# Optimization experiments

Hardware: AMD Instinct MI355X
Metric: run time of the kernel (lower is better)

## Reference

```python
import jax, jax.numpy as jnp
import numpy as np

B, S, H = 4, 1024, 1024
NH, HD = 16, 64          # heads, head_dim (NH*HD == H)
E, K, I = 8, 2, 1024     # routed experts, top_k, expert intermediate
NSH = 2                  # shared experts -> shared intermediate = NSH*I
EPS = 1e-6


def setup_inputs() -> dict:
    key = jax.random.key(0)
    ks = jax.random.split(key, 12)
    init = lambda k, shape: (jax.random.normal(k, shape, jnp.float32) * 0.02)
    return {
        "hidden_states": jax.random.normal(ks[0], (B, S, H), jnp.float32),
        "conditioning": jax.random.normal(ks[1], (B, H), jnp.float32),
        "adaLN_W": init(ks[2], (H, 6 * H)),
        "ln1_scale": jnp.ones((H,), jnp.float32),
        "ln1_bias": jnp.zeros((H,), jnp.float32),
        "ln2_scale": jnp.ones((H,), jnp.float32),
        "ln2_bias": jnp.zeros((H,), jnp.float32),
        "Wq": init(ks[3], (H, H)),
        "Wk": init(ks[4], (H, H)),
        "Wv": init(ks[5], (H, H)),
        "Wo": init(ks[6], (H, H)),
        "gate_kernel": init(ks[7], (E, H)),
        "We1": init(ks[8], (E, H, I)),
        "We2": init(ks[9], (E, I, H)),
        "Ws1": init(ks[10], (H, NSH * I)),
        "Ws2": init(ks[11], (NSH * I, H)),
    }


def _layernorm(x, scale, bias):
    m = x.mean(-1, keepdims=True)
    v = x.var(-1, keepdims=True)
    return (x - m) * jax.lax.rsqrt(v + EPS) * scale + bias


def _modulate(x, shift, scale):
    # (1 + scale) * x + shift, broadcasting [B,H] conditioning over seq dim
    return x * (1.0 + scale[:, None, :]) + shift[:, None, :]


def _attention(x, Wq, Wk, Wv, Wo):
    b, s, h = x.shape
    q = (x @ Wq).reshape(b, s, NH, HD)
    k = (x @ Wk).reshape(b, s, NH, HD)
    v = (x @ Wv).reshape(b, s, NH, HD)
    scores = jnp.einsum("bqnd,bknd->bnqk", q, k) / np.sqrt(HD).astype(np.float32)
    probs = jax.nn.softmax(scores, axis=-1)
    out = jnp.einsum("bnqk,bknd->bqnd", probs, v).reshape(b, s, h)
    return out @ Wo


def reference(hidden_states, conditioning, adaLN_W, ln1_scale, ln1_bias,
              ln2_scale, ln2_bias, Wq, Wk, Wv, Wo, gate_kernel, We1, We2,
              Ws1, Ws2):
    # adaLN modulation: SiLU -> Linear(H, 6H) -> chunk 6
    mods = jax.nn.silu(conditioning) @ adaLN_W  # [B, 6H]
    (shift_msa, scale_msa, gate_msa,
     shift_mlp, scale_mlp, gate_mlp) = jnp.split(mods, 6, axis=-1)

    normed = _modulate(_layernorm(hidden_states, ln1_scale, ln1_bias),
                       shift_msa, scale_msa)
    attn_out = _attention(normed, Wq, Wk, Wv, Wo)
    h = hidden_states + gate_msa[:, None, :] * attn_out

    normed2 = _modulate(_layernorm(h, ln2_scale, ln2_bias),
                        shift_mlp, scale_mlp)

    # --- MoE gate (DeepSeek-V2 style, greedy top-k, softmax scoring) ---
    logits = jnp.einsum("bsh,eh->bse", normed2.astype(jnp.float32),
                        gate_kernel.astype(jnp.float32))
    scores = jax.nn.softmax(logits, axis=-1)           # [B,S,E]
    topk_w, topk_idx = jax.lax.top_k(scores, K)        # [B,S,K]
    topk_w = topk_w / (topk_w.sum(-1, keepdims=True) + 1e-20)  # norm_topk_prob

    # --- dense all-expert MLPs then top-k combine (as in DiTMLPMoE) ---
    eh = jax.nn.gelu(jnp.einsum("bsh,ehi->ebsi", normed2, We1))  # [E,B,S,I]
    eo = jnp.einsum("ebsi,eih->bseh", eh, We2)                   # [B,S,E,H]
    sel = jnp.take_along_axis(eo, topk_idx[..., None], axis=2)   # [B,S,K,H]
    y = (sel * topk_w[..., None].astype(sel.dtype)).sum(axis=2)  # [B,S,H]

    # shared experts (always active)
    y = y + jax.nn.gelu(normed2 @ Ws1) @ Ws2

    return h + gate_mlp[:, None, :] * y
```

## Files before the change

kernel.cpp:

```cpp
#include <hip/hip_runtime.h>

typedef __bf16 bf16x8 __attribute__((ext_vector_type(8)));
typedef __bf16 bf16x4 __attribute__((ext_vector_type(4)));
typedef float  f32x4  __attribute__((ext_vector_type(4)));

__device__ inline float wred_sum(float v){
  #pragma unroll
  for (int d = 1; d < 64; d <<= 1) v += __shfl_xor(v, d, 64);
  return v;
}

__device__ inline float gelu_t(float x){
  const float c0 = 0.7978845608028654f;
  float t = tanhf(c0 * (x + 0.044715f * x * x * x));
  return 0.5f * x * (1.0f + t);
}

__device__ __forceinline__ void gload_lds16(const __bf16* g, __bf16* l){
  __builtin_amdgcn_global_load_lds((const __attribute__((address_space(1))) void*)g,
                                   (__attribute__((address_space(3))) void*)l, 16, 0, 0);
}

__global__ __launch_bounds__(256)
void transpose_cvt(const float* __restrict__ in, __bf16* __restrict__ out, int R, int C){
  long mo = (long)blockIdx.z * R * C;
  in += mo; out += mo;
  __shared__ float t[32][33];
  int r0 = blockIdx.y * 32, c0 = blockIdx.x * 32;
  int tid = threadIdx.x;
  int tr = tid >> 3, tc = (tid & 7) * 4;
  float4 vv = *(const float4*)&in[(long)(r0 + tr) * C + c0 + tc];
  t[tr][tc + 0] = vv.x; t[tr][tc + 1] = vv.y; t[tr][tc + 2] = vv.z; t[tr][tc + 3] = vv.w;
  __syncthreads();
  int oc = tid >> 3, orr = (tid & 7) * 4;
  bf16x4 o4;
  #pragma unroll
  for (int i = 0; i < 4; i++) o4[i] = (__bf16)t[orr + i][oc];
  *(bf16x4*)&out[(long)(c0 + oc) * R + r0 + orr] = o4;
}

__global__ __launch_bounds__(256)
void adaln_k(const float* __restrict__ cond, const float* __restrict__ W, float* __restrict__ mods){
  int b = blockIdx.y, z = blockIdx.z;
  int col = (blockIdx.x * 256 + threadIdx.x) * 4;
  __shared__ float sc[256];
  int h2 = z * 256 + threadIdx.x;
  float x = cond[b * 1024 + h2];
  sc[threadIdx.x] = x / (1.f + expf(-x));
  __syncthreads();
  float a0 = 0.f, a1 = 0.f, a2 = 0.f, a3 = 0.f;
  #pragma unroll 4
  for (int i = 0; i < 256; i++){
    float s = sc[i];
    float4 wv = *(const float4*)&W[(long)(z * 256 + i) * 6144 + col];
    a0 += s * wv.x; a1 += s * wv.y; a2 += s * wv.z; a3 += s * wv.w;
  }
  atomicAdd(&mods[b * 6144 + col + 0], a0);
  atomicAdd(&mods[b * 6144 + col + 1], a1);
  atomicAdd(&mods[b * 6144 + col + 2], a2);
  atomicAdd(&mods[b * 6144 + col + 3], a3);
}

__global__ __launch_bounds__(256)
void ln_mod(const float* __restrict__ x, const float* __restrict__ sc, const float* __restrict__ bi,
            const float* __restrict__ mods, int shift_off, int scale_off, __bf16* __restrict__ out){
  int row = blockIdx.x, tid = threadIdx.x, b = row >> 10;
  float4 xv = *(const float4*)&x[(long)row * 1024 + tid * 4];
  float s  = xv.x + xv.y + xv.z + xv.w;
  float s2 = xv.x * xv.x + xv.y * xv.y + xv.z * xv.z + xv.w * xv.w;
  s = wred_sum(s); s2 = wred_sum(s2);
  __shared__ float ssum[4], ssum2[4];
  int w = tid >> 6;
  if ((tid & 63) == 0){ ssum[w] = s; ssum2[w] = s2; }
  __syncthreads();
  s = ssum[0] + ssum[1] + ssum[2] + ssum[3];
  s2 = ssum2[0] + ssum2[1] + ssum2[2] + ssum2[3];
  float mean = s * (1.f / 1024.f);
  float var  = s2 * (1.f / 1024.f) - mean * mean;
  float inv  = rsqrtf(var + 1e-6f);
  const float xa[4] = {xv.x, xv.y, xv.z, xv.w};
  #pragma unroll
  for (int i = 0; i < 4; i++){
    int c = tid * 4 + i;
    float nv = (xa[i] - mean) * inv * sc[c] + bi[c];
    nv = nv * (1.f + mods[b * 6144 + scale_off + c]) + mods[b * 6144 + shift_off + c];
    out[(long)row * 1024 + c] = (__bf16)nv;
  }
}

__global__ __launch_bounds__(256)
void gate_k(const float* __restrict__ h, const float* __restrict__ ln2s, const float* __restrict__ ln2b,
            const float* __restrict__ mods, const float* __restrict__ gw,
            int* __restrict__ eidx, float* __restrict__ wpair){
  __shared__ float gws[8192];
  int tid = threadIdx.x;
  #pragma unroll
  for (int i = 0; i < 8; i++){
    int idx = tid + i * 256;
    *(float4*)&gws[idx * 4] = *(const float4*)&gw[idx * 4];
  }
  __syncthreads();
  int wv = tid >> 6, lane = tid & 63;
  int tok = blockIdx.x * 4 + wv;
  int b = tok >> 10;
  float4 xv[4]; float s = 0.f, s2 = 0.f;
  #pragma unroll
  for (int ch = 0; ch < 4; ch++){
    float4 v = *(const float4*)&h[(long)tok * 1024 + ch * 256 + lane * 4];
    xv[ch] = v;
    s  += v.x + v.y + v.z + v.w;
    s2 += v.x * v.x + v.y * v.y + v.z * v.z + v.w * v.w;
  }
  s = wred_sum(s); s2 = wred_sum(s2);
  float mean = s * (1.f / 1024.f);
  float var  = s2 * (1.f / 1024.f) - mean * mean;
  float inv  = rsqrtf(var + 1e-6f);
  float lg[8];
  #pragma unroll
  for (int e = 0; e < 8; e++) lg[e] = 0.f;
  #pragma unroll
  for (int ch = 0; ch < 4; ch++){
    int c = ch * 256 + lane * 4;
    float4 s4  = *(const float4*)&ln2s[c];
    float4 b4  = *(const float4*)&ln2b[c];
    float4 sc4 = *(const float4*)&mods[b * 6144 + 4096 + c];
    float4 sh4 = *(const float4*)&mods[b * 6144 + 3072 + c];
    float n0 = ((xv[ch].x - mean) * inv * s4.x + b4.x) * (1.f + sc4.x) + sh4.x;
    float n1 = ((xv[ch].y - mean) * inv * s4.y + b4.y) * (1.f + sc4.y) + sh4.y;
    float n2 = ((xv[ch].z - mean) * inv * s4.z + b4.z) * (1.f + sc4.z) + sh4.z;
    float n3 = ((xv[ch].w - mean) * inv * s4.w + b4.w) * (1.f + sc4.w) + sh4.w;
    #pragma unroll
    for (int e = 0; e < 8; e++){
      float4 g4 = *(const float4*)&gws[e * 1024 + c];
      lg[e] += n0 * g4.x + n1 * g4.y + n2 * g4.z + n3 * g4.w;
    }
  }
  #pragma unroll
  for (int e = 0; e < 8; e++) lg[e] = wred_sum(lg[e]);
  if (lane == 0){
    float mx = lg[0];
    #pragma unroll
    for (int e = 1; e < 8; e++) mx = fmaxf(mx, lg[e]);
    float p[8], ss = 0.f;
    #pragma unroll
    for (int e = 0; e < 8; e++){ p[e] = expf(lg[e] - mx); ss += p[e]; }
    #pragma unroll
    for (int e = 0; e < 8; e++) p[e] /= ss;
    int i0 = 0; float b0 = p[0];
    #pragma unroll
    for (int e = 1; e < 8; e++) if (p[e] > b0){ b0 = p[e]; i0 = e; }
    int i1 = -1; float b1 = -1.f;
    #pragma unroll
    for (int e = 0; e < 8; e++) if (e != i0 && p[e] > b1){ b1 = p[e]; i1 = e; }
    float dn = b0 + b1 + 1e-20f;
    eidx[tok * 2]     = i0; wpair[tok * 2]     = b0 / dn;
    eidx[tok * 2 + 1] = i1; wpair[tok * 2 + 1] = b1 / dn;
  }
}

__global__ __launch_bounds__(256)
void build_k(const int* __restrict__ eidx, int* __restrict__ counts, int* __restrict__ lists){
  int e = blockIdx.x;
  int tid = threadIdx.x, wv = tid >> 6, lane = tid & 63;
  __shared__ int base;
  __shared__ int woff[4];
  if (tid == 0) base = 0;
  __syncthreads();
  for (int it = 0; it < 32; ++it){
    int i = it * 256 + tid;
    bool m = (eidx[i] == e);
    unsigned long long bal = __ballot(m);
    int prefix = __popcll(bal & ((1ull << lane) - 1ull));
    if (lane == 0) woff[wv] = __popcll(bal);
    __syncthreads();
    int off = base;
    #pragma unroll
    for (int k = 0; k < 4; k++) if (k < wv) off += woff[k];
    if (m) lists[e * 4096 + off + prefix] = i;
    __syncthreads();
    if (tid == 0) base += woff[0] + woff[1] + woff[2] + woff[3];
    __syncthreads();
  }
  if (tid == 0) counts[e] = base;
}

__global__ __launch_bounds__(256)
void attn_k(const __bf16* __restrict__ qkv, __bf16* __restrict__ og){
  int bh = blockIdx.y; int bb = bh >> 4, hn = bh & 15;
  int q0 = blockIdx.x * 64;
  long tokbase = (long)bb * 1024;
  int hd0 = hn * 64;
  int tid = threadIdx.x; int w = tid >> 6; int lane = tid & 63;

  __shared__ __bf16 Ks[64][72];
  __shared__ __bf16 Vt[64][72];
  __shared__ __bf16 Ps[4][16][72];

  long qrow = tokbase + q0 + w * 16 + (lane & 15);
  bf16x8 qf0 = *(const bf16x8*)&qkv[qrow * 3072 + hd0 + (lane >> 4) * 8];
  bf16x8 qf1 = *(const bf16x8*)&qkv[qrow * 3072 + hd0 + 32 + (lane >> 4) * 8];
  #pragma unroll
  for (int i = 0; i < 8; i++){
    qf0[i] = (__bf16)((float)qf0[i] * 0.125f);
    qf1[i] = (__bf16)((float)qf1[i] * 0.125f);
  }

  float m_r[4], l_r[4];
  f32x4 oa[4];
  #pragma unroll
  for (int r = 0; r < 4; r++){ m_r[r] = -1e30f; l_r[r] = 0.f; }
  #pragma unroll
  for (int hb = 0; hb < 4; hb++) oa[hb] = (f32x4){0.f, 0.f, 0.f, 0.f};

  int dcol = tid & 63, rblk = tid >> 6;
  for (int t = 0; t < 16; t++){
    long kvbase = tokbase + t * 64;
    #pragma unroll
    for (int p = 0; p < 2; p++){
      int r = (tid >> 3) + p * 32;
      int c = (tid & 7) * 8;
      *(bf16x8*)&Ks[r][c] = *(const bf16x8*)&qkv[(kvbase + r) * 3072 + 1024 + hd0 + c];
    }
    bf16x8 col0, col1;
    #pragma unroll
    for (int i = 0; i < 8; i++)
      col0[i] = qkv[(kvbase + rblk * 16 + i) * 3072 + 2048 + hd0 + dcol];
    #pragma unroll
    for (int i = 0; i < 8; i++)
      col1[i] = qkv[(kvbase + rblk * 16 + 8 + i) * 3072 + 2048 + hd0 + dcol];
    *(bf16x8*)&Vt[dcol][rblk * 16]     = col0;
    *(bf16x8*)&Vt[dcol][rblk * 16 + 8] = col1;
    __syncthreads();
    f32x4 sf[4];
    #pragma unroll
    for (int cb = 0; cb < 4; cb++){
      bf16x8 kf0 = *(const bf16x8*)&Ks[cb * 16 + (lane & 15)][(lane >> 4) * 8];
      bf16x8 kf1 = *(const bf16x8*)&Ks[cb * 16 + (lane & 15)][32 + (lane >> 4) * 8];
      f32x4 sacc = (f32x4){0.f, 0.f, 0.f, 0.f};
      sacc = __builtin_amdgcn_mfma_f32_16x16x32_bf16(qf0, kf0, sacc, 0, 0, 0);
      sacc = __builtin_amdgcn_mfma_f32_16x16x32_bf16(qf1, kf1, sacc, 0, 0, 0);
      sf[cb] = sacc;
    }
    #pragma unroll
    for (int r = 0; r < 4; r++){
      float mx = fmaxf(fmaxf(sf[0][r], sf[1][r]), fmaxf(sf[2][r], sf[3][r]));
      #pragma unroll
      for (int d = 1; d < 16; d <<= 1) mx = fmaxf(mx, __shfl_xor(mx, d, 64));
      float mn = fmaxf(m_r[r], mx);
      float fr = expf(m_r[r] - mn);
      m_r[r] = mn;
      float ps = 0.f;
      #pragma unroll
      for (int cb = 0; cb < 4; cb++){
        float pe = expf(sf[cb][r] - mn);
        sf[cb][r] = pe;
        ps += pe;
      }
      #pragma unroll
      for (int d = 1; d < 16; d <<= 1) ps += __shfl_xor(ps, d, 64);
      l_r[r] = l_r[r] * fr + ps;
      #pragma unroll
      for (int hb = 0; hb < 4; hb++) oa[hb][r] *= fr;
    }
    #pragma unroll
    for (int cb = 0; cb < 4; cb++)
      #pragma unroll
      for (int r = 0; r < 4; r++)
        Ps[w][(lane >> 4) * 4 + r][cb * 16 + (lane & 15)] = (__bf16)sf[cb][r];
    __syncthreads();
    bf16x8 pf0 = *(const bf16x8*)&Ps[w][lane & 15][(lane >> 4) * 8];
    bf16x8 pf1 = *(const bf16x8*)&Ps[w][lane & 15][32 + (lane >> 4) * 8];
    #pragma unroll
    for (int hb = 0; hb < 4; hb++){
      bf16x8 vf0 = *(const bf16x8*)&Vt[hb * 16 + (lane & 15)][(lane >> 4) * 8];
      bf16x8 vf1 = *(const bf16x8*)&Vt[hb * 16 + (lane & 15)][32 + (lane >> 4) * 8];
      oa[hb] = __builtin_amdgcn_mfma_f32_16x16x32_bf16(pf0, vf0, oa[hb], 0, 0, 0);
      oa[hb] = __builtin_amdgcn_mfma_f32_16x16x32_bf16(pf1, vf1, oa[hb], 0, 0, 0);
    }
    __syncthreads();
  }
  #pragma unroll
  for (int hb = 0; hb < 4; hb++)
    #pragma unroll
    for (int r = 0; r < 4; r++){
      long row = tokbase + q0 + w * 16 + (lane >> 4) * 4 + r;
      float val = oa[hb][r] / l_r[r];
      og[row * 1024 + hd0 + hb * 16 + (lane & 15)] = (__bf16)val;
    }
}

template<int EPI, int GMODE>
__global__ __launch_bounds__(256)
void gemm_k(const __bf16* __restrict__ A, int lda,
            const __bf16* __restrict__ Bt, int K, long bstride,
            const int* __restrict__ lists, const int* __restrict__ counts,
            __bf16* __restrict__ outb, int ldo,
            float* __restrict__ outf,
            const float* __restrict__ resid,
            const float* __restrict__ mods, int mod_off,
            const float* __restrict__ wpair){
  int e = blockIdx.z;
  int cnt = 1 << 30;
  const int* list = nullptr;
  if (GMODE){
    cnt = counts[e];
    if ((int)blockIdx.y * 128 >= cnt) return;
    list = lists + e * 4096;
    Bt += (long)e * bstride;
  }
  int row0 = blockIdx.y * 128;
  int n0 = blockIdx.x * 128;
  int tid = threadIdx.x;
  int lane = tid & 63, w = tid >> 6;
  int wr = (w >> 1) * 64, wc = (w & 1) * 64;

  __shared__ __bf16 As[128 * 64];
  __shared__ __bf16 Bs[128 * 64];

  f32x4 acc[4][4];
  #pragma unroll
  for (int m = 0; m < 4; m++)
    #pragma unroll
    for (int n = 0; n < 4; n++) acc[m][n] = (f32x4){0.f, 0.f, 0.f, 0.f};

  long aoff[4]; const __bf16* bptr[4];
  #pragma unroll
  for (int j = 0; j < 4; j++){
    int r = w * 32 + j * 8 + (lane >> 3);
    int scb = (lane & 7) ^ (r & 7);
    int gr = row0 + r;
    int srcr;
    if (GMODE == 0) srcr = gr;
    else if (gr < cnt){ int pv = list[gr]; srcr = (GMODE == 1) ? (pv >> 1) : pv; }
    else { int pv = list[0]; srcr = (GMODE == 1) ? (pv >> 1) : pv; }
    aoff[j] = (long)srcr * lda + scb * 8;
    bptr[j] = Bt + (long)(n0 + r) * K + scb * 8;
  }
  const int nk = K / 64;
  for (int kt = 0; kt < nk; ++kt){
    int k0 = kt * 64;
    #pragma unroll
    for (int j = 0; j < 4; j++){
      gload_lds16(A + aoff[j] + k0, &As[(w * 32 + j * 8) * 64]);
      gload_lds16(bptr[j] + k0,     &Bs[(w * 32 + j * 8) * 64]);
    }
    __syncthreads();
    #pragma unroll
    for (int ks = 0; ks < 2; ++ks){
      bf16x8 af[4], bfr[4];
      #pragma unroll
      for (int m = 0; m < 4; m++){
        int r = wr + m * 16 + (lane & 15);
        int blk = (ks * 4 + (lane >> 4)) ^ (r & 7);
        af[m] = *(const bf16x8*)&As[r * 64 + blk * 8];
      }
      #pragma unroll
      for (int n = 0; n < 4; n++){
        int r = wc + n * 16 + (lane & 15);
        int blk = (ks * 4 + (lane >> 4)) ^ (r & 7);
        bfr[n] = *(const bf16x8*)&Bs[r * 64 + blk * 8];
      }
      #pragma unroll
      for (int m = 0; m < 4; m++)
        #pragma unroll
        for (int n = 0; n < 4; n++)
          acc[m][n] = __builtin_amdgcn_mfma_f32_16x16x32_bf16(af[m], bfr[n], acc[m][n], 0, 0, 0);
    }
    __syncthreads();
  }
  #pragma unroll
  for (int m = 0; m < 4; m++){
    #pragma unroll
    for (int r = 0; r < 4; r++){
      int rl = wr + m * 16 + (lane >> 4) * 4 + r;
      int grow = row0 + rl;
      if (GMODE && grow >= cnt) continue;
      #pragma unroll
      for (int n = 0; n < 4; n++){
        int col = n0 + wc + n * 16 + (lane & 15);
        float v = acc[m][n][r];
        if (EPI == 0){
          outb[(long)grow * ldo + col] = (__bf16)v;
        } else if (EPI == 1){
          int dst = (GMODE == 1) ? list[grow] : grow;
          outb[(long)dst * ldo + col] = (__bf16)gelu_t(v);
        } else if (EPI == 2){
          int b = grow >> 10;
          outf[(long)grow * 1024 + col] = resid[(long)grow * 1024 + col] + mods[b * 6144 + mod_off + col] * v;
        } else if (EPI == 3){
          outf[(long)grow * 1024 + col] = v;
        } else if (EPI == 4){
          int pv = list[grow];
          atomicAdd(&outf[(long)(pv >> 1) * 1024 + col], wpair[pv] * v);
        }
      }
    }
  }
}

__global__ __launch_bounds__(256)
void final_k(const float* __restrict__ h, const float* __restrict__ y,
             const float* __restrict__ mods, float* __restrict__ out){
  int i = blockIdx.x * 256 + threadIdx.x;
  long base = (long)i * 4;
  int row = (int)(base >> 10); int b = row >> 10; int c = (int)(base & 1023);
  float4 hv = *(const float4*)&h[base];
  float4 yv = *(const float4*)&y[base];
  const float* g = &mods[b * 6144 + 5120 + c];
  float4 o;
  o.x = hv.x + g[0] * yv.x;
  o.y = hv.y + g[1] * yv.y;
  o.z = hv.z + g[2] * yv.z;
  o.w = hv.w + g[3] * yv.w;
  *(float4*)&out[base] = o;
}

extern "C" void kernel_launch(void* const* d_in, const int* in_sizes, int n_in,
                              void* d_out, int out_size, void* d_ws, size_t ws_size,
                              hipStream_t stream){
  const float* hidden = (const float*)d_in[0];
  const float* cond   = (const float*)d_in[1];
  const float* adaW   = (const float*)d_in[2];
  const float* ln1s   = (const float*)d_in[3];
  const float* ln1b   = (const float*)d_in[4];
  const float* ln2s   = (const float*)d_in[5];
  const float* ln2b   = (const float*)d_in[6];
  const float* Wq     = (const float*)d_in[7];
  const float* Wk     = (const float*)d_in[8];
  const float* Wv     = (const float*)d_in[9];
  const float* Wo     = (const float*)d_in[10];
  const float* gatek  = (const float*)d_in[11];
  const float* We1    = (const float*)d_in[12];
  const float* We2    = (const float*)d_in[13];
  const float* Ws1    = (const float*)d_in[14];
  const float* Ws2    = (const float*)d_in[15];
  float* out = (float*)d_out;

  const size_t MB = 1024 * 1024;
  char* W = (char*)d_ws;
  size_t off = 0;
  auto take = [&](size_t b) -> void* {
    void* p = W + off;
    off += (b + 255) & ~((size_t)255);
    return p;
  };
  float*  mods   = (float*) take(4 * 6144 * sizeof(float));
  __bf16* qkvT   = (__bf16*)take(6 * MB);
  __bf16* WoT    = (__bf16*)take(2 * MB);
  __bf16* Ws1T   = (__bf16*)take(4 * MB);
  __bf16* Ws2T   = (__bf16*)take(4 * MB);
  __bf16* We1T   = (__bf16*)take(16 * MB);
  __bf16* We2T   = (__bf16*)take(16 * MB);
  __bf16* n1     = (__bf16*)take(8 * MB);
  __bf16* ab     = (__bf16*)take(8 * MB);
  __bf16* qkv    = (__bf16*)take(24 * MB);
  float*  hb     = (float*) take(16 * MB);
  __bf16* n2     = (__bf16*)take(8 * MB);
  float*  yb     = (float*) take(16 * MB);
  int*    counts = (int*)   take(256);
  int*    lists  = (int*)   take(8 * 4096 * 4);
  float*  wpair  = (float*) take(8192 * 4);
  int*    eidx   = (int*)   take(8192 * 4);
  __bf16* EH = n1;
  __bf16* SH = qkv;

  dim3 blk(256);

  hipMemsetAsync(mods, 0, 4 * 6144 * sizeof(float), stream);

  transpose_cvt<<<dim3(32, 32, 1), blk, 0, stream>>>(Wq,  qkvT,              1024, 1024);
  transpose_cvt<<<dim3(32, 32, 1), blk, 0, stream>>>(Wk,  qkvT + 1024*1024,  1024, 1024);
  transpose_cvt<<<dim3(32, 32, 1), blk, 0, stream>>>(Wv,  qkvT + 2048*1024,  1024, 1024);
  transpose_cvt<<<dim3(32, 32, 1), blk, 0, stream>>>(Wo,  WoT,  1024, 1024);
  transpose_cvt<<<dim3(64, 32, 1), blk, 0, stream>>>(Ws1, Ws1T, 1024, 2048);
  transpose_cvt<<<dim3(32, 64, 1), blk, 0, stream>>>(Ws2, Ws2T, 2048, 1024);
  transpose_cvt<<<dim3(32, 32, 8), blk, 0, stream>>>(We1, We1T, 1024, 1024);
  transpose_cvt<<<dim3(32, 32, 8), blk, 0, stream>>>(We2, We2T, 1024, 1024);

  adaln_k<<<dim3(6, 4, 4), blk, 0, stream>>>(cond, adaW, mods);

  ln_mod<<<4096, blk, 0, stream>>>(hidden, ln1s, ln1b, mods, 0, 1024, n1);

  gemm_k<0, 0><<<dim3(24, 32, 1), blk, 0, stream>>>(n1, 1024, qkvT, 1024, 0, nullptr, nullptr, qkv, 3072, nullptr, nullptr, nullptr, 0, nullptr);

  attn_k<<<dim3(16, 64, 1), blk, 0, stream>>>(qkv, ab);

  gemm_k<2, 0><<<dim3(8, 32, 1), blk, 0, stream>>>(ab, 1024, WoT, 1024, 0, nullptr, nullptr, nullptr, 0, hb, hidden, mods, 2048, nullptr);

  ln_mod<<<4096, blk, 0, stream>>>(hb, ln2s, ln2b, mods, 3072, 4096, n2);

  gate_k<<<1024, blk, 0, stream>>>(hb, ln2s, ln2b, mods, gatek, eidx, wpair);
  build_k<<<8, blk, 0, stream>>>(eidx, counts, lists);

  gemm_k<1, 0><<<dim3(16, 32, 1), blk, 0, stream>>>(n2, 1024, Ws1T, 1024, 0, nullptr, nullptr, SH, 2048, nullptr, nullptr, nullptr, 0, nullptr);
  gemm_k<3, 0><<<dim3(8, 32, 1), blk, 0, stream>>>(SH, 2048, Ws2T, 2048, 0, nullptr, nullptr, nullptr, 0, yb, nullptr, nullptr, 0, nullptr);

  gemm_k<1, 1><<<dim3(8, 32, 8), blk, 0, stream>>>(n2, 1024, We1T, 1024, 1048576, lists, counts, EH, 1024, nullptr, nullptr, nullptr, 0, nullptr);
  gemm_k<4, 2><<<dim3(8, 32, 8), blk, 0, stream>>>(EH, 1024, We2T, 1024, 1048576, lists, counts, nullptr, 0, yb, nullptr, nullptr, 0, wpair);

  final_k<<<4096, blk, 0, stream>>>(hb, yb, mods, out);

  (void)in_sizes; (void)n_in; (void)out_size; (void)ws_size;
}
```

Measured before the change: 582.3 us.

## Process 128 query rows per attention block with lazy softmax rescaling

The attention kernel now handles two 64-row query sub-tiles per block, so each K/V tile loaded into shared memory is reused twice. The grid is halved to match. Softmax uses exp2 with the log2e factor folded into the Q scale, and skips the running-max rescale when no row's max grows by more than a threshold. Row sums are accumulated with an MFMA against a ones vector, and the intra-iteration __syncthreads is removed because each wave owns its own P buffer. The block count is halved and register pressure rises, and the lazy rescale can leave unnormalised values up to 2^8 in bf16.

```diff
diff --git a/kernel.cpp b/kernel.cpp
--- a/kernel.cpp
+++ b/kernel.cpp
@@ -187,30 +187,43 @@
 __global__ __launch_bounds__(256)
 void attn_k(const __bf16* __restrict__ qkv, __bf16* __restrict__ og){
   int bh = blockIdx.y; int bb = bh >> 4, hn = bh & 15;
-  int q0 = blockIdx.x * 64;
+  int q0 = blockIdx.x * 128;
   long tokbase = (long)bb * 1024;
   int hd0 = hn * 64;
   int tid = threadIdx.x; int w = tid >> 6; int lane = tid & 63;
 
-  __shared__ __bf16 Ks[64][72];
-  __shared__ __bf16 Vt[64][72];
-  __shared__ __bf16 Ps[4][16][72];
-
-  long qrow = tokbase + q0 + w * 16 + (lane & 15);
-  bf16x8 qf0 = *(const bf16x8*)&qkv[qrow * 3072 + hd0 + (lane >> 4) * 8];
-  bf16x8 qf1 = *(const bf16x8*)&qkv[qrow * 3072 + hd0 + 32 + (lane >> 4) * 8];
-  #pragma unroll
-  for (int i = 0; i < 8; i++){
-    qf0[i] = (__bf16)((float)qf0[i] * 0.125f);
-    qf1[i] = (__bf16)((float)qf1[i] * 0.125f);
-  }
-
-  float m_r[4], l_r[4];
-  f32x4 oa[4];
-  #pragma unroll
-  for (int r = 0; r < 4; r++){ m_r[r] = -1e30f; l_r[r] = 0.f; }
-  #pragma unroll
-  for (int hb = 0; hb < 4; hb++) oa[hb] = (f32x4){0.f, 0.f, 0.f, 0.f};
+  __shared__ __bf16 Ks[64][76];
+  __shared__ __bf16 Vt[64][76];
+  __shared__ __bf16 Ps[4][32][76];
+
+  const float QS = 0.125f * 1.44269504088896f;
+  bf16x8 qf[2][2];
+  #pragma unroll
+  for (int sub = 0; sub < 2; sub++){
+    long qrow = tokbase + q0 + sub * 64 + w * 16 + (lane & 15);
+    qf[sub][0] = *(const bf16x8*)&qkv[qrow * 3072 + hd0 + (lane >> 4) * 8];
+    qf[sub][1] = *(const bf16x8*)&qkv[qrow * 3072 + hd0 + 32 + (lane >> 4) * 8];
+    #pragma unroll
+    for (int i = 0; i < 8; i++){
+      qf[sub][0][i] = (__bf16)((float)qf[sub][0][i] * QS);
+      qf[sub][1][i] = (__bf16)((float)qf[sub][1][i] * QS);
+    }
+  }
+
+  __bf16 one_b = (__bf16)1.0f;
+  bf16x8 one8 = (bf16x8){one_b, one_b, one_b, one_b, one_b, one_b, one_b, one_b};
+
+  float m_r[2][4];
+  f32x4 oa[2][4];
+  f32x4 lacc[2];
+  #pragma unroll
+  for (int sub = 0; sub < 2; sub++){
+    lacc[sub] = (f32x4){0.f, 0.f, 0.f, 0.f};
+    #pragma unroll
+    for (int r = 0; r < 4; r++) m_r[sub][r] = -1e30f;
+    #pragma unroll
+    for (int hb = 0; hb < 4; hb++) oa[sub][hb] = (f32x4){0.f, 0.f, 0.f, 0.f};
+  }
 
   int dcol = tid & 63, rblk = tid >> 6;
   for (int t = 0; t < 16; t++){
@@ -231,62 +244,76 @@
     *(bf16x8*)&Vt[dcol][rblk * 16]     = col0;
     *(bf16x8*)&Vt[dcol][rblk * 16 + 8] = col1;
     __syncthreads();
-    f32x4 sf[4];
-    #pragma unroll
-    for (int cb = 0; cb < 4; cb++){
-      bf16x8 kf0 = *(const bf16x8*)&Ks[cb * 16 + (lane & 15)][(lane >> 4) * 8];
-      bf16x8 kf1 = *(const bf16x8*)&Ks[cb * 16 + (lane & 15)][32 + (lane >> 4) * 8];
-      f32x4 sacc = (f32x4){0.f, 0.f, 0.f, 0.f};
-      sacc = __builtin_amdgcn_mfma_f32_16x16x32_bf16(qf0, kf0, sacc, 0, 0, 0);
-      sacc = __builtin_amdgcn_mfma_f32_16x16x32_bf16(qf1, kf1, sacc, 0, 0, 0);
-      sf[cb] = sacc;
-    }
-    #pragma unroll
-    for (int r = 0; r < 4; r++){
-      float mx = fmaxf(fmaxf(sf[0][r], sf[1][r]), fmaxf(sf[2][r], sf[3][r]));
-      #pragma unroll
-      for (int d = 1; d < 16; d <<= 1) mx = fmaxf(mx, __shfl_xor(mx, d, 64));
-      float mn = fmaxf(m_r[r], mx);
-      float fr = expf(m_r[r] - mn);
-      m_r[r] = mn;
-      float ps = 0.f;
+
+    #pragma unroll
+    for (int sub = 0; sub < 2; sub++){
+      f32x4 sf[4];
       #pragma unroll
       for (int cb = 0; cb < 4; cb++){
-        float pe = expf(sf[cb][r] - mn);
-        sf[cb][r] = pe;
-        ps += pe;
-      }
-      #pragma unroll
-      for (int d = 1; d < 16; d <<= 1) ps += __shfl_xor(ps, d, 64);
-      l_r[r] = l_r[r] * fr + ps;
-      #pragma unroll
-      for (int hb = 0; hb < 4; hb++) oa[hb][r] *= fr;
-    }
-    #pragma unroll
-    for (int cb = 0; cb < 4; cb++)
-      #pragma unroll
-      for (int r = 0; r < 4; r++)
-        Ps[w][(lane >> 4) * 4 + r][cb * 16 + (lane & 15)] = (__bf16)sf[cb][r];
-    __syncthreads();
-    bf16x8 pf0 = *(const bf16x8*)&Ps[w][lane & 15][(lane >> 4) * 8];
-    bf16x8 pf1 = *(const bf16x8*)&Ps[w][lane & 15][32 + (lane >> 4) * 8];
+        bf16x8 kf0 = *(const bf16x8*)&Ks[cb * 16 + (lane & 15)][(lane >> 4) * 8];
+        bf16x8 kf1 = *(const bf16x8*)&Ks[cb * 16 + (lane & 15)][32 + (lane >> 4) * 8];
+        f32x4 sacc = (f32x4){0.f, 0.f, 0.f, 0.f};
+        sacc = __builtin_amdgcn_mfma_f32_16x16x32_bf16(qf[sub][0], kf0, sacc, 0, 0, 0);
+        sacc = __builtin_amdgcn_mfma_f32_16x16x32_bf16(qf[sub][1], kf1, sacc, 0, 0, 0);
+        sf[cb] = sacc;
+      }
+      float mxr[4]; float dmax = -1e30f;
+      #pragma unroll
+      for (int r = 0; r < 4; r++){
+        float mx = fmaxf(fmaxf(sf[0][r], sf[1][r]), fmaxf(sf[2][r], sf[3][r]));
+        #pragma unroll
+        for (int d = 1; d < 16; d <<= 1) mx = fmaxf(mx, __shfl_xor(mx, d, 64));
+        mxr[r] = mx;
+        dmax = fmaxf(dmax, mx - m_r[sub][r]);
+      }
+      if (!__all(dmax <= 8.f)){
+        #pragma unroll
+        for (int r = 0; r < 4; r++){
+          float mn = fmaxf(m_r[sub][r], mxr[r]);
+          float fr = __builtin_amdgcn_exp2f(m_r[sub][r] - mn);
+          m_r[sub][r] = mn;
+          lacc[sub][r] *= fr;
+          #pragma unroll
+          for (int hb = 0; hb < 4; hb++) oa[sub][hb][r] *= fr;
+        }
+      }
+      #pragma unroll
+      for (int cb = 0; cb < 4; cb++)
+        #pragma unroll
+        for (int r = 0; r < 4; r++)
+          Ps[w][sub * 16 + (lane >> 4) * 4 + r][cb * 16 + (lane & 15)] =
+            (__bf16)__builtin_amdgcn_exp2f(sf[cb][r] - m_r[sub][r]);
+    }
+    bf16x8 pf[2][2];
+    #pragma unroll
+    for (int sub = 0; sub < 2; sub++){
+      pf[sub][0] = *(const bf16x8*)&Ps[w][sub * 16 + (lane & 15)][(lane >> 4) * 8];
+      pf[sub][1] = *(const bf16x8*)&Ps[w][sub * 16 + (lane & 15)][32 + (lane >> 4) * 8];
+      lacc[sub] = __builtin_amdgcn_mfma_f32_16x16x32_bf16(pf[sub][0], one8, lacc[sub], 0, 0, 0);
+      lacc[sub] = __builtin_amdgcn_mfma_f32_16x16x32_bf16(pf[sub][1], one8, lacc[sub], 0, 0, 0);
+    }
     #pragma unroll
     for (int hb = 0; hb < 4; hb++){
       bf16x8 vf0 = *(const bf16x8*)&Vt[hb * 16 + (lane & 15)][(lane >> 4) * 8];
       bf16x8 vf1 = *(const bf16x8*)&Vt[hb * 16 + (lane & 15)][32 + (lane >> 4) * 8];
-      oa[hb] = __builtin_amdgcn_mfma_f32_16x16x32_bf16(pf0, vf0, oa[hb], 0, 0, 0);
-      oa[hb] = __builtin_amdgcn_mfma_f32_16x16x32_bf16(pf1, vf1, oa[hb], 0, 0, 0);
-    }
-    __syncthreads();
-  }
-  #pragma unroll
-  for (int hb = 0; hb < 4; hb++)
-    #pragma unroll
-    for (int r = 0; r < 4; r++){
-      long row = tokbase + q0 + w * 16 + (lane >> 4) * 4 + r;
-      float val = oa[hb][r] / l_r[r];
-      og[row * 1024 + hd0 + hb * 16 + (lane & 15)] = (__bf16)val;
-    }
+      #pragma unroll
+      for (int sub = 0; sub < 2; sub++){
+        oa[sub][hb] = __builtin_amdgcn_mfma_f32_16x16x32_bf16(pf[sub][0], vf0, oa[sub][hb], 0, 0, 0);
+        oa[sub][hb] = __builtin_amdgcn_mfma_f32_16x16x32_bf16(pf[sub][1], vf1, oa[sub][hb], 0, 0, 0);
+      }
+    }
+    __syncthreads();
+  }
+  #pragma unroll
+  for (int sub = 0; sub < 2; sub++)
+    #pragma unroll
+    for (int hb = 0; hb < 4; hb++)
+      #pragma unroll
+      for (int r = 0; r < 4; r++){
+        long row = tokbase + q0 + sub * 64 + w * 16 + (lane >> 4) * 4 + r;
+        float val = oa[sub][hb][r] / lacc[sub][r];
+        og[row * 1024 + hd0 + hb * 16 + (lane & 15)] = (__bf16)val;
+      }
 }
 
 template<int EPI, int GMODE>
@@ -483,7 +510,7 @@
 
   gemm_k<0, 0><<<dim3(24, 32, 1), blk, 0, stream>>>(n1, 1024, qkvT, 1024, 0, nullptr, nullptr, qkv, 3072, nullptr, nullptr, nullptr, 0, nullptr);
 
-  attn_k<<<dim3(16, 64, 1), blk, 0, stream>>>(qkv, ab);
+  attn_k<<<dim3(8, 64, 1), blk, 0, stream>>>(qkv, ab);
 
   gemm_k<2, 0><<<dim3(8, 32, 1), blk, 0, stream>>>(ab, 1024, WoT, 1024, 0, nullptr, nullptr, nullptr, 0, hb, hidden, mods, 2048, nullptr);
 
```

Measured after the change: 561.7 us. 3.5% less time.
